# Performance work log

Measured on AMD Instinct MI355X. Metric: run time of the kernel, lower is better.

Reference implementation:

```python
import jax, jax.numpy as jnp
import numpy as np

B, A, C = 128, 8732, 21
ALPHA = 1.0
NEG_POS_RATIO = 3


def setup_inputs() -> dict:
    key = jax.random.key(0)
    k1, k2, k3, k4, k5 = jax.random.split(key, 5)
    confidences = jax.random.normal(k1, (B, A, C), dtype=jnp.float32)
    locations = jax.random.normal(k2, (B, A, 4), dtype=jnp.float32)
    gt_locations = jax.random.normal(k3, (B, A, 4), dtype=jnp.float32)
    raw_cls = jax.random.randint(k4, (B, A), 1, C)
    is_pos = jax.random.uniform(k5, (B, A)) < 0.03
    gt_labels = jnp.where(is_pos, raw_cls, 0).astype(jnp.int32)
    return {
        "confidences": confidences,
        "locations": locations,
        "gt_labels": gt_labels,
        "gt_locations": gt_locations,
    }


def reference(confidences, locations, gt_labels, gt_locations):
    pos_mask = gt_labels > 0                     # (B, A)
    neg_avail = gt_labels == 0                   # (B, A)

    # smooth L1 (beta=1) summed over positive anchors
    d = locations - gt_locations                 # (B, A, 4)
    ad = jnp.abs(d)
    sl1 = jnp.where(ad < 1.0, 0.5 * d * d, ad - 0.5)
    loc_loss = jnp.sum(sl1 * pos_mask[..., None].astype(sl1.dtype))

    # per-anchor cross entropy
    logp = jax.nn.log_softmax(confidences, axis=-1)              # (B, A, C)
    ce = -jnp.take_along_axis(logp, gt_labels[..., None].astype(jnp.int32), axis=-1)[..., 0]  # (B, A)

    # hard negative mining: top-(3*num_pos) CE among negatives, per row
    num_pos = jnp.sum(pos_mask, axis=1)                          # (B,)
    num_neg = jnp.minimum(NEG_POS_RATIO * num_pos, jnp.sum(neg_avail, axis=1))
    ce_neg = jnp.where(pos_mask, 0.0, ce)                        # zero out positives (CE >= 0)
    order = jnp.argsort(-ce_neg, axis=1)                         # descending
    ranks = jnp.argsort(order, axis=1)                           # rank of each anchor in descending order
    neg_mask = ranks < num_neg[:, None]

    keep = pos_mask | neg_mask
    conf_loss = jnp.sum(jnp.where(keep, ce, 0.0))

    total_loss = (loc_loss + ALPHA * conf_loss) / jnp.sum(num_pos).astype(loc_loss.dtype)
    return total_loss
```

## Files before the change

kernel.cpp:

```cpp
#include <hip/hip_runtime.h>
#include <math.h>

#define B_ 128
#define A_ 8732
#define C_ 21
#define APB 256
#define NBLK ((A_ + APB - 1) / APB)
#define NPART (B_ * NBLK)
#define KPT 9

typedef float f4 __attribute__((ext_vector_type(4)));

#define OFF_PLOC 0
#define OFF_PPCE 17920
#define OFF_PNP  35840
#define OFF_SCAL 53760
#define OFF_CEN  57344

__global__ __launch_bounds__(256) void k_ce(
        const float* __restrict__ conf, const float* __restrict__ loc,
        const int* __restrict__ lab, const float* __restrict__ gloc,
        float* __restrict__ ce_neg, float* __restrict__ part_loc,
        float* __restrict__ part_pce, int* __restrict__ part_np,
        float* __restrict__ gsum, int* __restrict__ gN,
        int* __restrict__ gticket)
{
    __shared__ float sConf[APB * C_];
    const int b   = blockIdx.y;
    const int a0  = blockIdx.x * APB;
    const int n   = min(APB, A_ - a0);
    const int tid = threadIdx.x;

    if (b == 0 && blockIdx.x == 0 && tid == 0) { *gsum = 0.f; *gN = 0; *gticket = 0; }

    const int a = a0 + min(tid, n - 1);
    const int L = lab[(size_t)b * A_ + a];

    {
        const size_t base = ((size_t)b * A_ + a0) * C_;
        const int n4 = (n * C_) >> 2;
        const f4* src4 = (const f4*)(conf + base);
        f4* dst4 = (f4*)sConf;
        #pragma unroll
        for (int j = 0; j < 6; j++) {
            const int i = tid + j * 256;
            if (i < n4) dst4[i] = src4[i];
        }
    }
    __syncthreads();

    float pce = 0.f, lloss = 0.f;
    int pcnt = 0;
    if (tid < n) {
        float v[C_];
        #pragma unroll
        for (int j = 0; j < C_; j++) v[j] = sConf[tid * C_ + j];
        float m = v[0];
        #pragma unroll
        for (int j = 1; j < C_; j++) m = fmaxf(m, v[j]);
        float s = 0.f;
        #pragma unroll
        for (int j = 0; j < C_; j++) s += __expf(v[j] - m);
        const float ce = __logf(s) + m - v[L];
        const bool pos = (L > 0);
        ce_neg[(size_t)b * A_ + a] = pos ? 0.f : ce;
        if (pos) {
            pce = ce;
            pcnt = 1;
            const float4 lv = ((const float4*)loc)[(size_t)b * A_ + a];
            const float4 gv = ((const float4*)gloc)[(size_t)b * A_ + a];
            float dx = lv.x - gv.x, dy = lv.y - gv.y, dz = lv.z - gv.z, dw = lv.w - gv.w;
            float ax = fabsf(dx), ay = fabsf(dy), az = fabsf(dz), aw = fabsf(dw);
            lloss  = (ax < 1.f) ? 0.5f * dx * dx : ax - 0.5f;
            lloss += (ay < 1.f) ? 0.5f * dy * dy : ay - 0.5f;
            lloss += (az < 1.f) ? 0.5f * dz * dz : az - 0.5f;
            lloss += (aw < 1.f) ? 0.5f * dw * dw : aw - 0.5f;
        }
    }

    #pragma unroll
    for (int off = 32; off > 0; off >>= 1) {
        pce   += __shfl_down(pce, off);
        lloss += __shfl_down(lloss, off);
        pcnt  += __shfl_down(pcnt, off);
    }
    __shared__ float wf[4], wl[4];
    __shared__ int wc[4];
    const int wave = tid >> 6, lane = tid & 63;
    if (lane == 0) { wf[wave] = pce; wl[wave] = lloss; wc[wave] = pcnt; }
    __syncthreads();
    if (tid == 0) {
        const int bid = b * NBLK + blockIdx.x;
        part_loc[bid] = wl[0] + wl[1] + wl[2] + wl[3];
        part_pce[bid] = wf[0] + wf[1] + wf[2] + wf[3];
        part_np[bid]  = wc[0] + wc[1] + wc[2] + wc[3];
    }
}

__global__ __launch_bounds__(1024, 2) void k_select(
        const float* __restrict__ ce_neg, const float* __restrict__ part_loc,
        const float* __restrict__ part_pce, const int* __restrict__ part_np,
        float* __restrict__ gsum, int* __restrict__ gN,
        int* __restrict__ gticket, float* __restrict__ out)
{
    const int b = blockIdx.x;
    const int tid = threadIdx.x;
    const int wave = tid >> 6, lane = tid & 63;

    __shared__ unsigned long long shCnt[2][16];
    __shared__ float shS[16];
    __shared__ int shNp;

    float contrib = 0.f;

    if (b == 128) {
        float s = 0.f; int n = 0;
        for (int i = tid; i < NPART; i += 1024) {
            s += part_loc[i] + part_pce[i];
            n += part_np[i];
        }
        #pragma unroll
        for (int off = 32; off > 0; off >>= 1) {
            s += __shfl_down(s, off);
            n += __shfl_down(n, off);
        }
        __shared__ int shN2[16];
        if (lane == 0) { shS[wave] = s; shN2[wave] = n; }
        __syncthreads();
        if (tid == 0) {
            float S = 0.f; int N = 0;
            #pragma unroll
            for (int w = 0; w < 16; w++) { S += shS[w]; N += shN2[w]; }
            contrib = S;
            atomicAdd(gN, N);
        }
    } else {
        const float* ce = ce_neg + (size_t)b * A_;

        unsigned keys[KPT];
        #pragma unroll
        for (int j = 0; j < KPT; j++) {
            const int i = tid + j * 1024;
            keys[j] = (i < A_) ? __float_as_uint(ce[i]) : 0u;
        }

        if (wave == 0) {
            int v = (lane < NBLK) ? part_np[b * NBLK + lane] : 0;
            #pragma unroll
            for (int off = 32; off > 0; off >>= 1) v += __shfl_down(v, off);
            if (lane == 0) shNp = v;
        }

        {
            unsigned c0 = 0; float s0 = 0.f;
            #pragma unroll
            for (int j = 0; j < KPT; j++) {
                c0 += (unsigned)__popcll(__ballot(keys[j] != 0u));
                s0 += __uint_as_float(keys[j]);
            }
            #pragma unroll
            for (int off = 32; off > 0; off >>= 1) s0 += __shfl_down(s0, off);
            if (lane == 0) { shCnt[0][wave] = c0; shS[wave] = s0; }
        }
        __syncthreads();

        const int np = shNp;
        const int k = min(3 * np, A_ - np);
        unsigned cnt0 = 0; float sum0 = 0.f;
        #pragma unroll
        for (int w = 0; w < 16; w++) { cnt0 += (unsigned)shCnt[0][w]; sum0 += shS[w]; }

        if (k <= 0) {
            contrib = 0.f;
        } else if (cnt0 < (unsigned)k) {
            contrib = sum0;
        } else {
            unsigned lo = 0u, hi = 0x42800000u;
            int p = 1;
            while (hi - lo > 1u) {
                const unsigned w = hi - lo;
                unsigned m1, m2, m3;
                if (w >= 4u) { const unsigned q = w >> 2; m1 = lo + q; m2 = lo + 2*q; m3 = lo + 3*q; }
                else         { m1 = m2 = m3 = lo + (w >> 1); }
                unsigned c1 = 0, c2 = 0, c3 = 0;
                #pragma unroll
                for (int j = 0; j < KPT; j++) {
                    c1 += (unsigned)__popcll(__ballot(keys[j] > m1));
                    c2 += (unsigned)__popcll(__ballot(keys[j] > m2));
                    c3 += (unsigned)__popcll(__ballot(keys[j] > m3));
                }
                if (lane == 0)
                    shCnt[p][wave] = (unsigned long long)c1
                                   | ((unsigned long long)c2 << 16)
                                   | ((unsigned long long)c3 << 32);
                __syncthreads();
                unsigned long long t = 0;
                #pragma unroll
                for (int w2 = 0; w2 < 16; w2++) t += shCnt[p][w2];
                const int C1 = (int)(t & 0xFFFF), C2 = (int)((t >> 16) & 0xFFFF),
                          C3 = (int)((t >> 32) & 0xFFFF);
                if      (C3 >= k) { lo = m3; }
                else if (C2 >= k) { lo = m2; hi = m3; }
                else if (C1 >= k) { lo = m1; hi = m2; }
                else              { hi = m1; }
                p ^= 1;
            }

            const unsigned kth = hi;
            unsigned c = 0; float s = 0.f;
            #pragma unroll
            for (int j = 0; j < KPT; j++) {
                c += (unsigned)__popcll(__ballot(keys[j] > kth));
                s += (keys[j] > kth) ? __uint_as_float(keys[j]) : 0.f;
            }
            #pragma unroll
            for (int off = 32; off > 0; off >>= 1) s += __shfl_down(s, off);
            if (lane == 0) { shCnt[0][wave] = c; shS[wave] = s; }
            __syncthreads();
            if (tid == 0) {
                unsigned Cg = 0; float Sg = 0.f;
                #pragma unroll
                for (int w = 0; w < 16; w++) { Cg += (unsigned)shCnt[0][w]; Sg += shS[w]; }
                contrib = Sg + (float)(k - (int)Cg) * __uint_as_float(kth);
            }
        }
    }

    if (tid == 0) {
        atomicAdd(gsum, contrib);
        __threadfence();
        const int t = atomicAdd(gticket, 1);
        if (t == 128) {
            const float S = atomicAdd(gsum, 0.f);
            const int   N = atomicAdd(gN, 0);
            out[0] = S / (float)N;
        }
    }
}

extern "C" void kernel_launch(void* const* d_in, const int* in_sizes, int n_in,
                              void* d_out, int out_size, void* d_ws, size_t ws_size,
                              hipStream_t stream) {
    const float* conf = (const float*)d_in[0];
    const float* loc  = (const float*)d_in[1];
    const int*   lab  = (const int*)d_in[2];
    const float* gloc = (const float*)d_in[3];

    char* ws = (char*)d_ws;
    float* part_loc = (float*)(ws + OFF_PLOC);
    float* part_pce = (float*)(ws + OFF_PPCE);
    int*   part_np  = (int*)(ws + OFF_PNP);
    float* gsum     = (float*)(ws + OFF_SCAL);
    int*   gN       = (int*)(ws + OFF_SCAL + 4);
    int*   gticket  = (int*)(ws + OFF_SCAL + 8);
    float* ce_neg   = (float*)(ws + OFF_CEN);

    dim3 g1(NBLK, B_);
    k_ce<<<g1, 256, 0, stream>>>(conf, loc, lab, gloc, ce_neg,
                                 part_loc, part_pce, part_np,
                                 gsum, gN, gticket);
    k_select<<<129, 1024, 0, stream>>>(ce_neg, part_loc, part_pce, part_np,
                                       gsum, gN, gticket, (float*)d_out);
}
```

Before: 188.6 us.

## Fuse CE computation and hard-negative selection into one per-row kernel

Replaces the two-kernel pipeline with a single kernel that has one 1024-thread block per batch row. Each block reads its row's confidences directly into registers using unaligned vector loads, computes CE and smooth-L1, and keeps the negative keys in registers for the threshold bisection. This removes the ce_neg round trip through global memory, the partial-sum buffers and the second launch, and a hipMemsetAsync now resets the global accumulators. The cost is that the confidence stream is spread over only 128 blocks with strided, non-LDS-staged loads, which may leave much of the GPU idle and hold back memory throughput.

```diff
diff --git a/kernel.cpp b/kernel.cpp
--- a/kernel.cpp
+++ b/kernel.cpp
@@ -4,233 +4,185 @@
 #define B_ 128
 #define A_ 8732
 #define C_ 21
-#define APB 256
-#define NBLK ((A_ + APB - 1) / APB)
-#define NPART (B_ * NBLK)
+#define TPB 1024
 #define KPT 9
-
-typedef float f4 __attribute__((ext_vector_type(4)));
-
-#define OFF_PLOC 0
-#define OFF_PPCE 17920
-#define OFF_PNP  35840
-#define OFF_SCAL 53760
-#define OFF_CEN  57344
-
-__global__ __launch_bounds__(256) void k_ce(
+#define NT 9
+
+typedef float f4u __attribute__((ext_vector_type(4), aligned(4)));
+
+#define OFF_SCAL 0
+
+__global__ __launch_bounds__(1024) void k_fused(
         const float* __restrict__ conf, const float* __restrict__ loc,
         const int* __restrict__ lab, const float* __restrict__ gloc,
-        float* __restrict__ ce_neg, float* __restrict__ part_loc,
-        float* __restrict__ part_pce, int* __restrict__ part_np,
-        float* __restrict__ gsum, int* __restrict__ gN,
-        int* __restrict__ gticket)
-{
-    __shared__ float sConf[APB * C_];
-    const int b   = blockIdx.y;
-    const int a0  = blockIdx.x * APB;
-    const int n   = min(APB, A_ - a0);
-    const int tid = threadIdx.x;
-
-    if (b == 0 && blockIdx.x == 0 && tid == 0) { *gsum = 0.f; *gN = 0; *gticket = 0; }
-
-    const int a = a0 + min(tid, n - 1);
-    const int L = lab[(size_t)b * A_ + a];
-
-    {
-        const size_t base = ((size_t)b * A_ + a0) * C_;
-        const int n4 = (n * C_) >> 2;
-        const f4* src4 = (const f4*)(conf + base);
-        f4* dst4 = (f4*)sConf;
-        #pragma unroll
-        for (int j = 0; j < 6; j++) {
-            const int i = tid + j * 256;
-            if (i < n4) dst4[i] = src4[i];
-        }
-    }
-    __syncthreads();
-
-    float pce = 0.f, lloss = 0.f;
-    int pcnt = 0;
-    if (tid < n) {
-        float v[C_];
-        #pragma unroll
-        for (int j = 0; j < C_; j++) v[j] = sConf[tid * C_ + j];
-        float m = v[0];
-        #pragma unroll
-        for (int j = 1; j < C_; j++) m = fmaxf(m, v[j]);
-        float s = 0.f;
-        #pragma unroll
-        for (int j = 0; j < C_; j++) s += __expf(v[j] - m);
-        const float ce = __logf(s) + m - v[L];
-        const bool pos = (L > 0);
-        ce_neg[(size_t)b * A_ + a] = pos ? 0.f : ce;
-        if (pos) {
-            pce = ce;
-            pcnt = 1;
-            const float4 lv = ((const float4*)loc)[(size_t)b * A_ + a];
-            const float4 gv = ((const float4*)gloc)[(size_t)b * A_ + a];
-            float dx = lv.x - gv.x, dy = lv.y - gv.y, dz = lv.z - gv.z, dw = lv.w - gv.w;
-            float ax = fabsf(dx), ay = fabsf(dy), az = fabsf(dz), aw = fabsf(dw);
-            lloss  = (ax < 1.f) ? 0.5f * dx * dx : ax - 0.5f;
-            lloss += (ay < 1.f) ? 0.5f * dy * dy : ay - 0.5f;
-            lloss += (az < 1.f) ? 0.5f * dz * dz : az - 0.5f;
-            lloss += (aw < 1.f) ? 0.5f * dw * dw : aw - 0.5f;
-        }
-    }
-
-    #pragma unroll
-    for (int off = 32; off > 0; off >>= 1) {
-        pce   += __shfl_down(pce, off);
-        lloss += __shfl_down(lloss, off);
-        pcnt  += __shfl_down(pcnt, off);
-    }
-    __shared__ float wf[4], wl[4];
-    __shared__ int wc[4];
-    const int wave = tid >> 6, lane = tid & 63;
-    if (lane == 0) { wf[wave] = pce; wl[wave] = lloss; wc[wave] = pcnt; }
-    __syncthreads();
-    if (tid == 0) {
-        const int bid = b * NBLK + blockIdx.x;
-        part_loc[bid] = wl[0] + wl[1] + wl[2] + wl[3];
-        part_pce[bid] = wf[0] + wf[1] + wf[2] + wf[3];
-        part_np[bid]  = wc[0] + wc[1] + wc[2] + wc[3];
-    }
-}
-
-__global__ __launch_bounds__(1024, 2) void k_select(
-        const float* __restrict__ ce_neg, const float* __restrict__ part_loc,
-        const float* __restrict__ part_pce, const int* __restrict__ part_np,
         float* __restrict__ gsum, int* __restrict__ gN,
         int* __restrict__ gticket, float* __restrict__ out)
 {
-    const int b = blockIdx.x;
-    const int tid = threadIdx.x;
-    const int wave = tid >> 6, lane = tid & 63;
-
     __shared__ unsigned long long shCnt[2][16];
     __shared__ float shS[16];
-    __shared__ int shNp;
-
-    float contrib = 0.f;
-
-    if (b == 128) {
-        float s = 0.f; int n = 0;
-        for (int i = tid; i < NPART; i += 1024) {
-            s += part_loc[i] + part_pce[i];
-            n += part_np[i];
-        }
+    __shared__ float shL[16];
+    __shared__ int   shC[16];
+    __shared__ int   shNp;
+
+    const int b    = blockIdx.x;
+    const int tid  = threadIdx.x;
+    const int wave = tid >> 6, lane = tid & 63;
+    const size_t rowoff = (size_t)b * A_;
+
+    unsigned keys[KPT];
+    float pce = 0.f, lloss = 0.f;
+    int pcnt = 0;
+
+    #pragma unroll
+    for (int t = 0; t < NT; ++t) {
+        const int a  = t * TPB + tid;
+        unsigned key = 0u;
+        if (a < A_) {
+            const int L = lab[rowoff + a];
+
+            const float* vp = conf + (rowoff + a) * C_;
+            float v[C_];
+            #pragma unroll
+            for (int q = 0; q < 5; ++q) {
+                const f4u x = *(const f4u*)(vp + 4 * q);
+                v[4*q+0] = x.x; v[4*q+1] = x.y; v[4*q+2] = x.z; v[4*q+3] = x.w;
+            }
+            v[20] = vp[20];
+
+            float m = v[0];
+            #pragma unroll
+            for (int j = 1; j < C_; ++j) m = fmaxf(m, v[j]);
+            float s = 0.f;
+            #pragma unroll
+            for (int j = 0; j < C_; ++j) s += __expf(v[j] - m);
+
+            float vL = v[0];
+            #pragma unroll
+            for (int j = 1; j < C_; ++j) vL = (j == L) ? v[j] : vL;
+
+            const float ce = __logf(s) + m - vL;
+            if (L > 0) {
+                pce += ce;
+                pcnt++;
+                const float4 lv = ((const float4*)loc)[rowoff + a];
+                const float4 gv = ((const float4*)gloc)[rowoff + a];
+                float dx = lv.x - gv.x, dy = lv.y - gv.y,
+                      dz = lv.z - gv.z, dw = lv.w - gv.w;
+                float ax = fabsf(dx), ay = fabsf(dy),
+                      az = fabsf(dz), aw = fabsf(dw);
+                lloss += (ax < 1.f) ? 0.5f * dx * dx : ax - 0.5f;
+                lloss += (ay < 1.f) ? 0.5f * dy * dy : ay - 0.5f;
+                lloss += (az < 1.f) ? 0.5f * dz * dz : az - 0.5f;
+                lloss += (aw < 1.f) ? 0.5f * dw * dw : aw - 0.5f;
+            } else {
+                key = __float_as_uint(ce);
+            }
+        }
+        keys[t] = key;
+    }
+
+    {
+        float p = pce, l = lloss; int c = pcnt;
         #pragma unroll
         for (int off = 32; off > 0; off >>= 1) {
-            s += __shfl_down(s, off);
-            n += __shfl_down(n, off);
-        }
-        __shared__ int shN2[16];
-        if (lane == 0) { shS[wave] = s; shN2[wave] = n; }
+            p += __shfl_down(p, off);
+            l += __shfl_down(l, off);
+            c += __shfl_down(c, off);
+        }
+        if (lane == 0) { shS[wave] = p; shL[wave] = l; shC[wave] = c; }
+    }
+    __syncthreads();
+    float rowsum = 0.f;
+    if (tid == 0) {
+        float P = 0.f, Lx = 0.f; int Cc = 0;
+        #pragma unroll
+        for (int w = 0; w < 16; ++w) { P += shS[w]; Lx += shL[w]; Cc += shC[w]; }
+        shNp = Cc;
+        rowsum = P + Lx;
+    }
+    __syncthreads();
+    const int np = shNp;
+
+    {
+        unsigned c0 = 0; float s0 = 0.f;
+        #pragma unroll
+        for (int j = 0; j < KPT; ++j) {
+            c0 += (unsigned)__popcll(__ballot(keys[j] != 0u));
+            s0 += __uint_as_float(keys[j]);
+        }
+        #pragma unroll
+        for (int off = 32; off > 0; off >>= 1) s0 += __shfl_down(s0, off);
+        if (lane == 0) { shCnt[0][wave] = c0; shS[wave] = s0; }
+    }
+    __syncthreads();
+
+    const int k = min(3 * np, A_ - np);
+    unsigned cnt0 = 0; float sum0 = 0.f;
+    #pragma unroll
+    for (int w = 0; w < 16; ++w) { cnt0 += (unsigned)shCnt[0][w]; sum0 += shS[w]; }
+
+    float negsum = 0.f;
+    if (k <= 0) {
+        negsum = 0.f;
+    } else if (cnt0 < (unsigned)k) {
+        negsum = sum0;
+    } else {
+        unsigned lo = 0u, hi = 0x42800000u;
+        int p = 1;
+        while (hi - lo > 1u) {
+            const unsigned w = hi - lo;
+            unsigned m1, m2, m3;
+            if (w >= 4u) { const unsigned q = w >> 2; m1 = lo + q; m2 = lo + 2*q; m3 = lo + 3*q; }
+            else         { m1 = m2 = m3 = lo + (w >> 1); }
+            unsigned c1 = 0, c2 = 0, c3 = 0;
+            #pragma unroll
+            for (int j = 0; j < KPT; ++j) {
+                c1 += (unsigned)__popcll(__ballot(keys[j] > m1));
+                c2 += (unsigned)__popcll(__ballot(keys[j] > m2));
+                c3 += (unsigned)__popcll(__ballot(keys[j] > m3));
+            }
+            if (lane == 0)
+                shCnt[p][wave] = (unsigned long long)c1
+                               | ((unsigned long long)c2 << 16)
+                               | ((unsigned long long)c3 << 32);
+            __syncthreads();
+            unsigned long long tsum = 0;
+            #pragma unroll
+            for (int w2 = 0; w2 < 16; ++w2) tsum += shCnt[p][w2];
+            const int C1 = (int)(tsum & 0xFFFF), C2 = (int)((tsum >> 16) & 0xFFFF),
+                      C3 = (int)((tsum >> 32) & 0xFFFF);
+            if      (C3 >= k) { lo = m3; }
+            else if (C2 >= k) { lo = m2; hi = m3; }
+            else if (C1 >= k) { lo = m1; hi = m2; }
+            else              { hi = m1; }
+            p ^= 1;
+        }
+
+        const unsigned kth = hi;
+        unsigned c = 0; float s = 0.f;
+        #pragma unroll
+        for (int j = 0; j < KPT; ++j) {
+            c += (unsigned)__popcll(__ballot(keys[j] > kth));
+            s += (keys[j] > kth) ? __uint_as_float(keys[j]) : 0.f;
+        }
+        #pragma unroll
+        for (int off = 32; off > 0; off >>= 1) s += __shfl_down(s, off);
+        if (lane == 0) { shCnt[0][wave] = c; shS[wave] = s; }
         __syncthreads();
         if (tid == 0) {
-            float S = 0.f; int N = 0;
-            #pragma unroll
-            for (int w = 0; w < 16; w++) { S += shS[w]; N += shN2[w]; }
-            contrib = S;
-            atomicAdd(gN, N);
-        }
-    } else {
-        const float* ce = ce_neg + (size_t)b * A_;
-
-        unsigned keys[KPT];
-        #pragma unroll
-        for (int j = 0; j < KPT; j++) {
-            const int i = tid + j * 1024;
-            keys[j] = (i < A_) ? __float_as_uint(ce[i]) : 0u;
-        }
-
-        if (wave == 0) {
-            int v = (lane < NBLK) ? part_np[b * NBLK + lane] : 0;
-            #pragma unroll
-            for (int off = 32; off > 0; off >>= 1) v += __shfl_down(v, off);
-            if (lane == 0) shNp = v;
-        }
-
-        {
-            unsigned c0 = 0; float s0 = 0.f;
-            #pragma unroll
-            for (int j = 0; j < KPT; j++) {
-                c0 += (unsigned)__popcll(__ballot(keys[j] != 0u));
-                s0 += __uint_as_float(keys[j]);
-            }
-            #pragma unroll
-            for (int off = 32; off > 0; off >>= 1) s0 += __shfl_down(s0, off);
-            if (lane == 0) { shCnt[0][wave] = c0; shS[wave] = s0; }
-        }
-        __syncthreads();
-
-        const int np = shNp;
-        const int k = min(3 * np, A_ - np);
-        unsigned cnt0 = 0; float sum0 = 0.f;
-        #pragma unroll
-        for (int w = 0; w < 16; w++) { cnt0 += (unsigned)shCnt[0][w]; sum0 += shS[w]; }
-
-        if (k <= 0) {
-            contrib = 0.f;
-        } else if (cnt0 < (unsigned)k) {
-            contrib = sum0;
-        } else {
-            unsigned lo = 0u, hi = 0x42800000u;
-            int p = 1;
-            while (hi - lo > 1u) {
-                const unsigned w = hi - lo;
-                unsigned m1, m2, m3;
-                if (w >= 4u) { const unsigned q = w >> 2; m1 = lo + q; m2 = lo + 2*q; m3 = lo + 3*q; }
-                else         { m1 = m2 = m3 = lo + (w >> 1); }
-                unsigned c1 = 0, c2 = 0, c3 = 0;
-                #pragma unroll
-                for (int j = 0; j < KPT; j++) {
-                    c1 += (unsigned)__popcll(__ballot(keys[j] > m1));
-                    c2 += (unsigned)__popcll(__ballot(keys[j] > m2));
-                    c3 += (unsigned)__popcll(__ballot(keys[j] > m3));
-                }
-                if (lane == 0)
-                    shCnt[p][wave] = (unsigned long long)c1
-                                   | ((unsigned long long)c2 << 16)
-                                   | ((unsigned long long)c3 << 32);
-                __syncthreads();
-                unsigned long long t = 0;
-                #pragma unroll
-                for (int w2 = 0; w2 < 16; w2++) t += shCnt[p][w2];
-                const int C1 = (int)(t & 0xFFFF), C2 = (int)((t >> 16) & 0xFFFF),
-                          C3 = (int)((t >> 32) & 0xFFFF);
-                if      (C3 >= k) { lo = m3; }
-                else if (C2 >= k) { lo = m2; hi = m3; }
-                else if (C1 >= k) { lo = m1; hi = m2; }
-                else              { hi = m1; }
-                p ^= 1;
-            }
-
-            const unsigned kth = hi;
-            unsigned c = 0; float s = 0.f;
-            #pragma unroll
-            for (int j = 0; j < KPT; j++) {
-                c += (unsigned)__popcll(__ballot(keys[j] > kth));
-                s += (keys[j] > kth) ? __uint_as_float(keys[j]) : 0.f;
-            }
-            #pragma unroll
-            for (int off = 32; off > 0; off >>= 1) s += __shfl_down(s, off);
-            if (lane == 0) { shCnt[0][wave] = c; shS[wave] = s; }
-            __syncthreads();
-            if (tid == 0) {
-                unsigned Cg = 0; float Sg = 0.f;
-                #pragma unroll
-                for (int w = 0; w < 16; w++) { Cg += (unsigned)shCnt[0][w]; Sg += shS[w]; }
-                contrib = Sg + (float)(k - (int)Cg) * __uint_as_float(kth);
-            }
+            unsigned Cg = 0; float Sg = 0.f;
+            #pragma unroll
+            for (int w = 0; w < 16; ++w) { Cg += (unsigned)shCnt[0][w]; Sg += shS[w]; }
+            negsum = Sg + (float)(k - (int)Cg) * __uint_as_float(kth);
         }
     }
 
     if (tid == 0) {
-        atomicAdd(gsum, contrib);
+        atomicAdd(gsum, rowsum + negsum);
+        atomicAdd(gN, np);
         __threadfence();
         const int t = atomicAdd(gticket, 1);
-        if (t == 128) {
+        if (t == B_ - 1) {
             const float S = atomicAdd(gsum, 0.f);
             const int   N = atomicAdd(gN, 0);
             out[0] = S / (float)N;
@@ -247,18 +199,12 @@
     const float* gloc = (const float*)d_in[3];
 
     char* ws = (char*)d_ws;
-    float* part_loc = (float*)(ws + OFF_PLOC);
-    float* part_pce = (float*)(ws + OFF_PPCE);
-    int*   part_np  = (int*)(ws + OFF_PNP);
-    float* gsum     = (float*)(ws + OFF_SCAL);
-    int*   gN       = (int*)(ws + OFF_SCAL + 4);
-    int*   gticket  = (int*)(ws + OFF_SCAL + 8);
-    float* ce_neg   = (float*)(ws + OFF_CEN);
-
-    dim3 g1(NBLK, B_);
-    k_ce<<<g1, 256, 0, stream>>>(conf, loc, lab, gloc, ce_neg,
-                                 part_loc, part_pce, part_np,
-                                 gsum, gN, gticket);
-    k_select<<<129, 1024, 0, stream>>>(ce_neg, part_loc, part_pce, part_np,
-                                       gsum, gN, gticket, (float*)d_out);
+    float* gsum    = (float*)(ws + OFF_SCAL);
+    int*   gN      = (int*)(ws + OFF_SCAL + 4);
+    int*   gticket = (int*)(ws + OFF_SCAL + 8);
+
+    hipMemsetAsync(ws + OFF_SCAL, 0, 12, stream);
+
+    k_fused<<<B_, TPB, 0, stream>>>(conf, loc, lab, gloc,
+                                    gsum, gN, gticket, (float*)d_out);
 }
```

Measured after the change: 190.7 us. No clear change (+1.1%).
